# Kernel tuning notes

Measured on AMD Instinct MI355X. Metric: run time of the kernel, lower is better.

The kernel has to match this reference:

```python
import jax, jax.numpy as jnp
import numpy as np

N = 20000      # nodes per graph
E = 320000     # edges per graph (before self-loops)
G = 256        # graphs (strings) per side
VOCAB = 128    # NUMBER_EMBEDDINGS
D_IN = 128
HID = 64
H = 4
D_OUT = 128
NEG_SLOPE = 0.2  # PyG GATConv leaky_relu slope


def _gat(x, edge_index, W, att_s, att_d, bias, concat):
    """PyG GATConv: gather -> per-edge logits -> segment softmax over dst -> scatter.
    x: [N, F_in], W: [F_in, H*C], att_s/att_d: [H, C], bias: [H*C] or [C].
    Self-loops are added (PyG default add_self_loops=True)."""
    n = x.shape[0]
    h, c = att_s.shape
    loops = jnp.arange(n)
    src = jnp.concatenate([edge_index[0], loops])  # message sources j
    dst = jnp.concatenate([edge_index[1], loops])  # message targets i
    xh = (x @ W).reshape(n, h, c)                  # [N,H,C]
    a_s = jnp.einsum('nhc,hc->nh', xh, att_s)      # [N,H]
    a_d = jnp.einsum('nhc,hc->nh', xh, att_d)
    logits = jax.nn.leaky_relu(a_s[src] + a_d[dst], NEG_SLOPE)  # [E',H]
    m = jax.ops.segment_max(logits, dst, num_segments=n)
    m = jnp.where(jnp.isfinite(m), m, 0.0)
    e = jnp.exp(logits - m[dst])
    z = jax.ops.segment_sum(e, dst, num_segments=n)
    alpha = e / (z[dst] + 1e-16)                   # [E',H]
    msg = xh[src] * alpha[:, :, None]              # [E',H,C]
    out = jax.ops.segment_sum(msg, dst, num_segments=n)  # [N,H,C]
    out = out.reshape(n, h * c) if concat else out.mean(axis=1)
    return out + bias


def _encode(xi, ei, batch, emb, W1, as1, ad1, b1, lw1, lb1,
            W2, as2, ad2, b2, lw2, lb2, W3, as3, ad3, b3, lw3, lb3):
    e = emb[xi]  # [N, D_IN]
    x = jax.nn.relu(_gat(e, ei, W1, as1, ad1, b1, True) + e @ lw1 + lb1)
    x = jax.nn.relu(_gat(x, ei, W2, as2, ad2, b2, True) + x @ lw2 + lb2)
    x = _gat(x, ei, W3, as3, ad3, b3, False) + x @ lw3 + lb3  # [N, D_OUT]
    s = jax.ops.segment_sum(x, batch, num_segments=G)
    cnt = jax.ops.segment_sum(jnp.ones((x.shape[0],), x.dtype), batch, num_segments=G)
    return s / jnp.maximum(cnt, 1.0)[:, None]  # global_mean_pool -> [G, D_OUT]


def setup_inputs() -> dict:
    key = jax.random.key(0)
    ks = jax.random.split(key, 32)
    hc = H * HID  # 256
    def nrm(k, shape, scale=0.05):
        return jax.random.normal(k, shape, dtype=jnp.float32) * scale
    inp = {
        'x_l': jax.random.randint(ks[0], (N,), 0, VOCAB),
        'edge_l': jax.random.randint(ks[1], (2, E), 0, N),
        'batch_l': jnp.sort(jax.random.randint(ks[2], (N,), 0, G)),
        'x_r': jax.random.randint(ks[3], (N,), 0, VOCAB),
        'edge_r': jax.random.randint(ks[4], (2, E), 0, N),
        'batch_r': jnp.sort(jax.random.randint(ks[5], (N,), 0, G)),
        'emb': nrm(ks[6], (VOCAB, D_IN), 1.0),
        'W1': nrm(ks[7], (D_IN, hc)), 'as1': nrm(ks[8], (H, HID)), 'ad1': nrm(ks[9], (H, HID)),
        'b1': jnp.zeros((hc,), jnp.float32), 'lw1': nrm(ks[10], (D_IN, hc)), 'lb1': jnp.zeros((hc,), jnp.float32),
        'W2': nrm(ks[11], (hc, hc)), 'as2': nrm(ks[12], (H, HID)), 'ad2': nrm(ks[13], (H, HID)),
        'b2': jnp.zeros((hc,), jnp.float32), 'lw2': nrm(ks[14], (hc, hc)), 'lb2': jnp.zeros((hc,), jnp.float32),
        'W3': nrm(ks[15], (hc, H * D_OUT)), 'as3': nrm(ks[16], (H, D_OUT)), 'ad3': nrm(ks[17], (H, D_OUT)),
        'b3': jnp.zeros((D_OUT,), jnp.float32), 'lw3': nrm(ks[18], (hc, D_OUT)), 'lb3': jnp.zeros((D_OUT,), jnp.float32),
    }
    return inp


def reference(x_l, edge_l, batch_l, x_r, edge_r, batch_r, emb,
              W1, as1, ad1, b1, lw1, lb1,
              W2, as2, ad2, b2, lw2, lb2,
              W3, as3, ad3, b3, lw3, lb3):
    params = (emb, W1, as1, ad1, b1, lw1, lb1, W2, as2, ad2, b2, lw2, lb2,
              W3, as3, ad3, b3, lw3, lb3)
    out_l = _encode(x_l, edge_l, batch_l, *params)
    out_r = _encode(x_r, edge_r, batch_r, *params)
    return (out_l, out_r)
```

## Files before the change

kernel.cpp:

```cpp
#include <hip/hip_runtime.h>

#define GG 256

typedef __bf16 bf16x8 __attribute__((ext_vector_type(8)));
typedef __bf16 bf16x4 __attribute__((ext_vector_type(4)));
typedef float floatx4 __attribute__((ext_vector_type(4)));
typedef float f32x2 __attribute__((ext_vector_type(2)));

__device__ __forceinline__ float lrelu(float x) { return x > 0.f ? x : 0.2f * x; }

__device__ __forceinline__ int permM(int m) {
    int g = m >> 6, q = m & 63;
    return (g << 6) | ((q & 3) << 4) | (q >> 2);
}

__device__ __forceinline__ void wt1(const float* __restrict__ B, __bf16* __restrict__ Bt,
                                    int K, int M, int idx) {
    int k = idx / M, m = idx - k * M;
    Bt[(size_t)permM(m) * K + k] = (__bf16)B[idx];
}
__device__ __forceinline__ void wattn1(const float* __restrict__ W,
                                       const float* __restrict__ as_,
                                       const float* __restrict__ ad_,
                                       __bf16* __restrict__ dst, int K, int C, int idx) {
    int j = idx / K, k = idx - j * K;
    float v = 0.f;
    if (j < 8) {
        int h = j & 3;
        const float* att = (j < 4) ? as_ : ad_;
        int M = 4 * C;
        for (int c = 0; c < C; c++) v += W[(size_t)k * M + h * C + c] * att[h * C + c];
    }
    dst[(size_t)j * K + k] = (__bf16)v;
}

__global__ void k_wprep(const float* W1, const float* lw1, const float* as1, const float* ad1,
                        const float* W2, const float* lw2, const float* as2, const float* ad2,
                        const float* W3, const float* lw3, const float* as3, const float* ad3,
                        __bf16* B1t, __bf16* B2t, __bf16* B3t) {
    int idx = blockIdx.x * blockDim.x + threadIdx.x;
    if (idx < 32768) { wt1(W1, B1t, 128, 256, idx); return; }
    idx -= 32768;
    if (idx < 32768) { wt1(lw1, B1t + 256 * 128, 128, 256, idx); return; }
    idx -= 32768;
    if (idx < 2048) { wattn1(W1, as1, ad1, B1t + 512 * 128, 128, 64, idx); return; }
    idx -= 2048;
    if (idx < 65536) { wt1(W2, B2t, 256, 256, idx); return; }
    idx -= 65536;
    if (idx < 65536) { wt1(lw2, B2t + 256 * 256, 256, 256, idx); return; }
    idx -= 65536;
    if (idx < 4096) { wattn1(W2, as2, ad2, B2t + 512 * 256, 256, 64, idx); return; }
    idx -= 4096;
    if (idx < 131072) { wt1(W3, B3t, 256, 512, idx); return; }
    idx -= 131072;
    if (idx < 32768) { wt1(lw3, B3t + 512 * 256, 256, 128, idx); return; }
    idx -= 32768;
    if (idx < 4096) { wattn1(W3, as3, ad3, B3t + 640 * 256, 256, 128, idx); }
}

template <int K, bool EMB, bool LINBF>
__global__ __launch_bounds__(256) void k_gemm_all(const __bf16* __restrict__ A,
                                                  const int* __restrict__ xl,
                                                  const int* __restrict__ xr,
                                                  const float* __restrict__ emb,
                                                  const __bf16* __restrict__ Bt,
                                                  int n, int n1, int Mx, int Ml,
                                                  unsigned char* __restrict__ x8, int ldx,
                                                  float* __restrict__ linf,
                                                  __bf16* __restrict__ linb, int ldl,
                                                  const float* __restrict__ bias1,
                                                  const float* __restrict__ bias2,
                                                  float* __restrict__ a_s,
                                                  float* __restrict__ a_d) {
    constexpr int KS = K / 32;
    constexpr int LDK = K + 8;
    constexpr int LPR = K / 8;
    constexpr int NCH = 64 * LPR / 256;
    __shared__ __bf16 S[64 * LDK];
    int tid = threadIdx.x;
    int wave = tid >> 6, lane = tid & 63;
    int row0 = blockIdx.x * 64;
#pragma unroll
    for (int c = 0; c < NCH; c++) {
        int i = tid + c * 256;
        int r = i / LPR, ko = (i - r * LPR) * 8;
        int gr = row0 + r;
        bf16x8 v = {};
        if (gr < n) {
            if (EMB) {
                int xi = (gr < n1) ? xl[gr] : xr[gr - n1];
                const float4* src = (const float4*)(emb + ((size_t)xi << 7) + ko);
                float4 q0 = src[0], q1 = src[1];
                v = bf16x8{(__bf16)q0.x, (__bf16)q0.y, (__bf16)q0.z, (__bf16)q0.w,
                           (__bf16)q1.x, (__bf16)q1.y, (__bf16)q1.z, (__bf16)q1.w};
            } else {
                v = *(const bf16x8*)(A + (size_t)gr * K + ko);
            }
        }
        *(bf16x8*)&S[r * LDK + ko] = v;
    }
    __syncthreads();
    int kOff = (lane >> 4) * 8;
    int colBase = lane & 15;
    bf16x8 af[KS];
#pragma unroll
    for (int ks = 0; ks < KS; ks++)
        af[ks] = *(const bf16x8*)&S[(wave * 16 + colBase) * LDK + ks * 32 + kOff];
    int Mtot = Mx + Ml;
    int gr0 = row0 + wave * 16 + ((lane >> 4) << 2);
    int half = (Mtot / 128) * 64;
    int c0beg = blockIdx.y * half;
    int T = half / 64;
    bf16x8 regs[NCH];
#pragma unroll
    for (int c = 0; c < NCH; c++) {
        int i = tid + c * 256;
        int r = i / LPR, ko = (i - r * LPR) * 8;
        regs[c] = *(const bf16x8*)(Bt + (size_t)(c0beg + r) * K + ko);
    }
    for (int t = 0; t < T; t++) {
        __syncthreads();
#pragma unroll
        for (int c = 0; c < NCH; c++) {
            int i = tid + c * 256;
            int r = i / LPR, ko = (i - r * LPR) * 8;
            *(bf16x8*)&S[r * LDK + ko] = regs[c];
        }
        if (t + 1 < T) {
            int c0n = c0beg + (t + 1) * 64;
#pragma unroll
            for (int c = 0; c < NCH; c++) {
                int i = tid + c * 256;
                int r = i / LPR, ko = (i - r * LPR) * 8;
                regs[c] = *(const bf16x8*)(Bt + (size_t)(c0n + r) * K + ko);
            }
        }
        __syncthreads();
        floatx4 acc[4] = {};
#pragma unroll
        for (int ct = 0; ct < 4; ct++) {
#pragma unroll
            for (int ks = 0; ks < KS; ks++) {
                bf16x8 bf = *(const bf16x8*)&S[(ct * 16 + colBase) * LDK + ks * 32 + kOff];
                acc[ct] = __builtin_amdgcn_mfma_f32_16x16x32_bf16(af[ks], bf, acc[ct], 0, 0, 0);
            }
        }
        int c0 = c0beg + t * 64;
        if (c0 < Mx) {
#pragma unroll
            for (int r = 0; r < 4; r++) {
                int gr = gr0 + r;
                if (gr >= n) continue;
                int p = __builtin_amdgcn_cvt_pk_fp8_f32(acc[0][r], acc[1][r], 0, false);
                p = __builtin_amdgcn_cvt_pk_fp8_f32(acc[2][r], acc[3][r], p, true);
                *(unsigned int*)(x8 + (size_t)gr * ldx + c0 + colBase * 4) = (unsigned int)p;
            }
        } else {
            int c2 = c0 + colBase * 4 - Mx;
#pragma unroll
            for (int r = 0; r < 4; r++) {
                int gr = gr0 + r;
                if (gr >= n) continue;
                float v0 = acc[0][r] + bias1[c2 + 0];
                float v1 = acc[1][r] + bias1[c2 + 1];
                float v2 = acc[2][r] + bias1[c2 + 2];
                float v3 = acc[3][r] + bias1[c2 + 3];
                if (bias2) {
                    v0 += bias2[c2 + 0]; v1 += bias2[c2 + 1];
                    v2 += bias2[c2 + 2]; v3 += bias2[c2 + 3];
                }
                if (LINBF) {
                    bf16x4 o = {(__bf16)v0, (__bf16)v1, (__bf16)v2, (__bf16)v3};
                    *(bf16x4*)(linb + (size_t)gr * ldl + c2) = o;
                } else {
                    float4 o = {v0, v1, v2, v3};
                    *(float4*)(linf + (size_t)gr * ldl + c2) = o;
                }
            }
        }
    }
    if (blockIdx.y == 1) {
        floatx4 acc = {};
        const __bf16* bp = Bt + (size_t)(Mtot + colBase) * K + kOff;
#pragma unroll
        for (int ks = 0; ks < KS; ks++) {
            bf16x8 bf = *(const bf16x8*)(bp + ks * 32);
            acc = __builtin_amdgcn_mfma_f32_16x16x32_bf16(af[ks], bf, acc, 0, 0, 0);
        }
        if (colBase < 8) {
            float* dst = (colBase < 4) ? a_s : a_d;
            int h = colBase & 3;
#pragma unroll
            for (int r = 0; r < 4; r++) {
                int gr = gr0 + r;
                if (gr < n) dst[gr * 4 + h] = acc[r];
            }
        }
    }
}

__global__ void k_hist2(const int* __restrict__ el, const int* __restrict__ er,
                        int E, int n, int* __restrict__ deg) {
    int e = blockIdx.x * blockDim.x + threadIdx.x;
    if (e >= 2 * E) return;
    int d = (e < E) ? el[E + e] : er[E + (e - E)] + n;
    atomicAdd(&deg[d], 1);
}

__global__ __launch_bounds__(1024) void k_scan1(int* __restrict__ rp, int n,
                                                int* __restrict__ part) {
    __shared__ int wsum[16];
    int i = blockIdx.x * 1024 + threadIdx.x;
    int lane = threadIdx.x & 63, wid = threadIdx.x >> 6;
    int v = (i < n) ? rp[i] : 0;
    int inc = v;
#pragma unroll
    for (int off = 1; off < 64; off <<= 1) {
        int t = __shfl_up(inc, off, 64);
        if (lane >= off) inc += t;
    }
    if (lane == 63) wsum[wid] = inc;
    __syncthreads();
    if (wid == 0) {
        int wv = (lane < 16) ? wsum[lane] : 0;
        int winc = wv;
#pragma unroll
        for (int off = 1; off < 16; off <<= 1) {
            int t = __shfl_up(winc, off, 64);
            if (lane >= off) winc += t;
        }
        if (lane < 16) wsum[lane] = winc - wv;
        if (lane == 15) part[blockIdx.x] = winc;
    }
    __syncthreads();
    if (i < n) rp[i] = wsum[wid] + (inc - v);
}

__global__ void k_scan2(int* __restrict__ part, int nb) {
    int lane = threadIdx.x;
    int v = (lane < nb) ? part[lane] : 0;
    int inc = v;
#pragma unroll
    for (int off = 1; off < 64; off <<= 1) {
        int t = __shfl_up(inc, off, 64);
        if (lane >= off) inc += t;
    }
    if (lane < nb) part[lane] = inc - v;
}

__global__ __launch_bounds__(1024) void k_scan3(int* __restrict__ rp, int n,
                                                const int* __restrict__ part) {
    int i = blockIdx.x * 1024 + threadIdx.x;
    if (i < n) rp[i] += part[blockIdx.x];
}

__global__ void k_fill2(const int* __restrict__ el, const int* __restrict__ er,
                        int E, int n, int* __restrict__ rp, int* __restrict__ csr) {
    int e = blockIdx.x * blockDim.x + threadIdx.x;
    if (e >= 2 * E) return;
    int d, s;
    if (e < E) { s = el[e]; d = el[E + e]; }
    else       { s = er[e - E] + n; d = er[E + (e - E)] + n; }
    int pos = atomicAdd(&rp[d], 1);
    csr[pos] = s;
}

__device__ __forceinline__ void dec4(unsigned int u, float* f) {
    f32x2 a = __builtin_amdgcn_cvt_pk_f32_fp8(u, false);
    f32x2 b = __builtin_amdgcn_cvt_pk_f32_fp8(u, true);
    f[0] = a[0]; f[1] = a[1]; f[2] = b[0]; f[3] = b[1];
}

__device__ __forceinline__ int swz_block(int bid, int nbx) {
    if (nbx & 7) return bid;
    int halfb = nbx >> 1;
    int grp = bid >> 3, r = bid & 7;
    int j = grp * 4 + (r & 3);
    return (r < 4) ? j : halfb + j;
}

__global__ __launch_bounds__(256) void k_agg12(const int* __restrict__ rp,
                                               const int* __restrict__ csr,
                                               const float* __restrict__ a_s,
                                               const float* __restrict__ a_d,
                                               const unsigned char* __restrict__ x8,
                                               const __bf16* __restrict__ lin,
                                               __bf16* __restrict__ out_bf, int n) {
    int nb = swz_block(blockIdx.x, gridDim.x);
    int lane = threadIdx.x & 63;
    int half = lane >> 5, sl = lane & 31;
    int node = nb * 4 + (threadIdx.x >> 6);
    if (node >= n) return;
    int c0 = sl * 8;
    int h = sl >> 3;
    int start = node ? rp[node - 1] : 0;
    int end = rp[node];
    float ad = a_d[node * 4 + h];
    float z = 0.f;
    float acc[8] = {};
    if (half == 0) {
        z = __expf(lrelu(a_s[node * 4 + h] + ad));
        uint2 u = *(const uint2*)(x8 + (size_t)node * 256 + c0);
        float f[8];
        dec4(u.x, f); dec4(u.y, f + 4);
#pragma unroll
        for (int j = 0; j < 8; j++) acc[j] = z * f[j];
    }
    uint2 u0 = {}, u1 = {}, u2 = {};
    float A0 = 0.f, A1 = 0.f, A2 = 0.f;
    int e0 = start + half;
    if (e0 < end) {
        int s = csr[e0];
        u0 = *(const uint2*)(x8 + (size_t)s * 256 + c0);
        A0 = a_s[s * 4 + h];
    }
    if (e0 + 2 < end) {
        int s = csr[e0 + 2];
        u1 = *(const uint2*)(x8 + (size_t)s * 256 + c0);
        A1 = a_s[s * 4 + h];
    }
    if (e0 + 4 < end) {
        int s = csr[e0 + 4];
        u2 = *(const uint2*)(x8 + (size_t)s * 256 + c0);
        A2 = a_s[s * 4 + h];
    }
    for (int e = e0; e < end; e += 2) {
        uint2 uc = u0;
        float ac = A0;
        u0 = u1; A0 = A1;
        u1 = u2; A1 = A2;
        int pn = e + 6;
        pn = pn < end ? pn : end - 1;
        int s = csr[pn];
        u2 = *(const uint2*)(x8 + (size_t)s * 256 + c0);
        A2 = a_s[s * 4 + h];
        float w = __expf(lrelu(ac + ad));
        z += w;
        float f[8];
        dec4(uc.x, f); dec4(uc.y, f + 4);
#pragma unroll
        for (int q = 0; q < 8; q++) acc[q] += w * f[q];
    }
    z += __shfl_xor(z, 32, 64);
#pragma unroll
    for (int j = 0; j < 8; j++) acc[j] += __shfl_xor(acc[j], 32, 64);
    if (half == 0) {
        float inv = 1.f / (z + 1e-16f);
        bf16x8 l = *(const bf16x8*)(lin + (size_t)node * 256 + c0);
        bf16x8 r;
#pragma unroll
        for (int j = 0; j < 8; j++)
            r[j] = (__bf16)fmaxf(acc[j] * inv + (float)l[j], 0.f);
        *(bf16x8*)(out_bf + (size_t)node * 256 + c0) = r;
    }
}

__global__ __launch_bounds__(256) void k_agg3(const int* __restrict__ rp,
                                              const int* __restrict__ csr,
                                              const float* __restrict__ a_s,
                                              const float* __restrict__ a_d,
                                              const unsigned int* __restrict__ x8,
                                              float* __restrict__ mean, int n) {
    int nb = swz_block(blockIdx.x, gridDim.x);
    int lane = threadIdx.x & 63;
    int half = lane >> 5, sl = lane & 31;
    int node = nb * 4 + (threadIdx.x >> 6);
    if (node >= n) return;
    int h = sl >> 3;
    int start = node ? rp[node - 1] : 0;
    int end = rp[node];
    float ad = a_d[node * 4 + h];
    float z = 0.f;
    float acc[16] = {};
    if (half == 0) {
        z = __expf(lrelu(a_s[node * 4 + h] + ad));
        uint4 u = *(const uint4*)(x8 + (size_t)node * 128 + sl * 4);
        float f[16];
        dec4(u.x, f); dec4(u.y, f + 4); dec4(u.z, f + 8); dec4(u.w, f + 12);
#pragma unroll
        for (int j = 0; j < 16; j++) acc[j] = z * f[j];
    }
    uint4 u0 = {}, u1 = {}, u2 = {};
    float A0 = 0.f, A1 = 0.f, A2 = 0.f;
    int e0 = start + half;
    if (e0 < end) {
        int s = csr[e0];
        u0 = *(const uint4*)(x8 + (size_t)s * 128 + sl * 4);
        A0 = a_s[s * 4 + h];
    }
    if (e0 + 2 < end) {
        int s = csr[e0 + 2];
        u1 = *(const uint4*)(x8 + (size_t)s * 128 + sl * 4);
        A1 = a_s[s * 4 + h];
    }
    if (e0 + 4 < end) {
        int s = csr[e0 + 4];
        u2 = *(const uint4*)(x8 + (size_t)s * 128 + sl * 4);
        A2 = a_s[s * 4 + h];
    }
    for (int e = e0; e < end; e += 2) {
        uint4 uc = u0;
        float ac = A0;
        u0 = u1; A0 = A1;
        u1 = u2; A1 = A2;
        int pn = e + 6;
        pn = pn < end ? pn : end - 1;
        int s = csr[pn];
        u2 = *(const uint4*)(x8 + (size_t)s * 128 + sl * 4);
        A2 = a_s[s * 4 + h];
        float w = __expf(lrelu(ac + ad));
        z += w;
        float f[16];
        dec4(uc.x, f); dec4(uc.y, f + 4); dec4(uc.z, f + 8); dec4(uc.w, f + 12);
#pragma unroll
        for (int q = 0; q < 16; q++) acc[q] += w * f[q];
    }
    z += __shfl_xor(z, 32, 64);
#pragma unroll
    for (int j = 0; j < 16; j++) acc[j] += __shfl_xor(acc[j], 32, 64);
    float scale = 0.25f / (z + 1e-16f);
#pragma unroll
    for (int j = 0; j < 16; j++) {
        float v = acc[j] * scale;
        v += __shfl_xor(v, 8, 64);
        v += __shfl_xor(v, 16, 64);
        acc[j] = v;
    }
    if (lane < 8) {
        float4* op = (float4*)(mean + (size_t)node * 128 + lane * 16);
#pragma unroll
        for (int q = 0; q < 4; q++) {
            float4 o = {acc[4 * q], acc[4 * q + 1], acc[4 * q + 2], acc[4 * q + 3]};
            op[q] = o;
        }
    }
}

__global__ __launch_bounds__(128) void k_pool(const float* __restrict__ mean,
                                              const float* __restrict__ lin3,
                                              const float* __restrict__ b3,
                                              const int* __restrict__ bl,
                                              const int* __restrict__ br,
                                              int n, float* __restrict__ out) {
    int g = blockIdx.x, c = threadIdx.x;
    const int* b = (g < GG) ? bl : br;
    int tg = (g < GG) ? g : g - GG;
    int off = (g < GG) ? 0 : n;
    int s, e;
    { int lo = 0, hi = n; while (lo < hi) { int m = (lo + hi) >> 1; if (b[m] < tg) lo = m + 1; else hi = m; } s = lo; }
    { int lo = 0, hi = n; while (lo < hi) { int m = (lo + hi) >> 1; if (b[m] < tg + 1) lo = m + 1; else hi = m; } e = lo; }
    s += off; e += off;
    float acc = 0.f;
    for (int i = s; i < e; i++)
        acc += mean[(size_t)i * 128 + c] + lin3[(size_t)i * 128 + c];
    int cnt = e - s;
    out[(size_t)g * 128 + c] = cnt > 0 ? acc / (float)cnt + b3[c] : 0.f;
}

static inline int cdiv(int a, int b) { return (a + b - 1) / b; }

extern "C" void kernel_launch(void* const* d_in, const int* in_sizes, int n_in,
                              void* d_out, int out_size, void* d_ws, size_t ws_size,
                              hipStream_t stream) {
    const int* x_l = (const int*)d_in[0];
    const int* edge_l = (const int*)d_in[1];
    const int* batch_l = (const int*)d_in[2];
    const int* x_r = (const int*)d_in[3];
    const int* edge_r = (const int*)d_in[4];
    const int* batch_r = (const int*)d_in[5];
    const float* emb = (const float*)d_in[6];
    const float* W1 = (const float*)d_in[7];
    const float* as1 = (const float*)d_in[8];
    const float* ad1 = (const float*)d_in[9];
    const float* b1 = (const float*)d_in[10];
    const float* lw1 = (const float*)d_in[11];
    const float* lb1 = (const float*)d_in[12];
    const float* W2 = (const float*)d_in[13];
    const float* as2 = (const float*)d_in[14];
    const float* ad2 = (const float*)d_in[15];
    const float* b2 = (const float*)d_in[16];
    const float* lw2 = (const float*)d_in[17];
    const float* lb2 = (const float*)d_in[18];
    const float* W3 = (const float*)d_in[19];
    const float* as3 = (const float*)d_in[20];
    const float* ad3 = (const float*)d_in[21];
    const float* b3 = (const float*)d_in[22];
    const float* lw3 = (const float*)d_in[23];
    const float* lb3 = (const float*)d_in[24];

    const int n = in_sizes[0];
    const int E = in_sizes[1] / 2;
    const int N2 = 2 * n;
    const int NB = cdiv(N2, 1024);

    float* MEAN = (float*)d_ws;
    float* L3 = MEAN + (size_t)N2 * 128;
    float* a_s = L3 + (size_t)N2 * 128;
    float* a_d = a_s + (size_t)N2 * 4;
    int* rp = (int*)(a_d + (size_t)N2 * 4);
    int* csr = rp + N2;
    int* part = csr + 2 * E;
    __bf16* LINb = (__bf16*)(part + 64);
    unsigned char* X8a = (unsigned char*)(LINb + (size_t)N2 * 256);
    unsigned char* X8b = X8a + (size_t)N2 * 256;
    __bf16* Abf = (__bf16*)(X8b + (size_t)N2 * 512);
    __bf16* B1t = Abf + (size_t)N2 * 256;
    __bf16* B2t = B1t + 528 * 128;
    __bf16* B3t = B2t + 528 * 256;

    const int TB = 256;
    dim3 blk(TB);

    k_wprep<<<cdiv(370688, TB), blk, 0, stream>>>(W1, lw1, as1, ad1, W2, lw2, as2, ad2,
                                                  W3, lw3, as3, ad3, B1t, B2t, B3t);

    hipMemsetAsync(rp, 0, sizeof(int) * (size_t)N2, stream);
    k_hist2<<<cdiv(2 * E, TB), blk, 0, stream>>>(edge_l, edge_r, E, n, rp);
    k_scan1<<<NB, 1024, 0, stream>>>(rp, N2, part);
    k_scan2<<<1, 64, 0, stream>>>(part, NB);
    k_scan3<<<NB, 1024, 0, stream>>>(rp, N2, part);
    k_fill2<<<cdiv(2 * E, TB), blk, 0, stream>>>(edge_l, edge_r, E, n, rp, csr);

    k_gemm_all<128, true, true><<<dim3(cdiv(N2, 64), 2), blk, 0, stream>>>(
        nullptr, x_l, x_r, emb, B1t, N2, n, 256, 256, X8a, 256, nullptr, LINb, 256, lb1, b1, a_s, a_d);
    k_agg12<<<cdiv(N2, 4), blk, 0, stream>>>(rp, csr, a_s, a_d, X8a, LINb, Abf, N2);

    k_gemm_all<256, false, true><<<dim3(cdiv(N2, 64), 2), blk, 0, stream>>>(
        Abf, nullptr, nullptr, nullptr, B2t, N2, n, 256, 256, X8a, 256, nullptr, LINb, 256, lb2, b2, a_s, a_d);
    k_agg12<<<cdiv(N2, 4), blk, 0, stream>>>(rp, csr, a_s, a_d, X8a, LINb, Abf, N2);

    k_gemm_all<256, false, false><<<dim3(cdiv(N2, 64), 2), blk, 0, stream>>>(
        Abf, nullptr, nullptr, nullptr, B3t, N2, n, 512, 128, X8b, 512, L3, nullptr, 128, lb3, nullptr, a_s, a_d);
    k_agg3<<<cdiv(N2, 4), blk, 0, stream>>>(rp, csr, a_s, a_d, (const unsigned int*)X8b, MEAN, N2);
    k_pool<<<2 * GG, 128, 0, stream>>>(MEAN, L3, b3, batch_l, batch_r, n, (float*)d_out);
}
```

Measured before the change: 447.5 us.

## Double GEMM row tile to 128 and load A fragments directly from global

The fused GEMM now gives each block 128 rows instead of 64, so every wave holds two 16-row A fragments and reuses each B tile in shared memory across twice as many MFMAs. The A tile is read straight from global memory (or the embedding table) into registers, removing the shared-memory staging pass and its barrier. The aim is to halve B-tile global and LDS traffic per output row and to cut block count. The cost is higher register pressure from doubled accumulators and fragments, which may lower occupancy, and fewer blocks across the device.

Result: no change. 455.7 us (+1.8%).

```diff
diff --git a/kernel.cpp b/kernel.cpp
--- a/kernel.cpp
+++ b/kernel.cpp
@@ -79,35 +79,34 @@
     __shared__ __bf16 S[64 * LDK];
     int tid = threadIdx.x;
     int wave = tid >> 6, lane = tid & 63;
-    int row0 = blockIdx.x * 64;
-#pragma unroll
-    for (int c = 0; c < NCH; c++) {
-        int i = tid + c * 256;
-        int r = i / LPR, ko = (i - r * LPR) * 8;
-        int gr = row0 + r;
-        bf16x8 v = {};
-        if (gr < n) {
-            if (EMB) {
-                int xi = (gr < n1) ? xl[gr] : xr[gr - n1];
-                const float4* src = (const float4*)(emb + ((size_t)xi << 7) + ko);
-                float4 q0 = src[0], q1 = src[1];
-                v = bf16x8{(__bf16)q0.x, (__bf16)q0.y, (__bf16)q0.z, (__bf16)q0.w,
-                           (__bf16)q1.x, (__bf16)q1.y, (__bf16)q1.z, (__bf16)q1.w};
-            } else {
-                v = *(const bf16x8*)(A + (size_t)gr * K + ko);
-            }
-        }
-        *(bf16x8*)&S[r * LDK + ko] = v;
-    }
-    __syncthreads();
+    int row0 = blockIdx.x * 128;
     int kOff = (lane >> 4) * 8;
     int colBase = lane & 15;
-    bf16x8 af[KS];
-#pragma unroll
-    for (int ks = 0; ks < KS; ks++)
-        af[ks] = *(const bf16x8*)&S[(wave * 16 + colBase) * LDK + ks * 32 + kOff];
+
+    bf16x8 af[2][KS];
+#pragma unroll
+    for (int as = 0; as < 2; as++) {
+        int row = row0 + wave * 32 + as * 16 + colBase;
+        row = row < n ? row : (n - 1);
+        if (EMB) {
+            int xi = (row < n1) ? xl[row] : xr[row - n1];
+            const float* src = emb + ((size_t)xi << 7);
+#pragma unroll
+            for (int ks = 0; ks < KS; ks++) {
+                const float4* p = (const float4*)(src + ks * 32 + kOff);
+                float4 q0 = p[0], q1 = p[1];
+                af[as][ks] = bf16x8{(__bf16)q0.x, (__bf16)q0.y, (__bf16)q0.z, (__bf16)q0.w,
+                                    (__bf16)q1.x, (__bf16)q1.y, (__bf16)q1.z, (__bf16)q1.w};
+            }
+        } else {
+            const __bf16* src = A + (size_t)row * K;
+#pragma unroll
+            for (int ks = 0; ks < KS; ks++)
+                af[as][ks] = *(const bf16x8*)(src + ks * 32 + kOff);
+        }
+    }
+
     int Mtot = Mx + Ml;
-    int gr0 = row0 + wave * 16 + ((lane >> 4) << 2);
     int half = (Mtot / 128) * 64;
     int c0beg = blockIdx.y * half;
     int T = half / 64;
@@ -136,64 +135,72 @@
             }
         }
         __syncthreads();
-        floatx4 acc[4] = {};
+        floatx4 acc[2][4] = {};
 #pragma unroll
         for (int ct = 0; ct < 4; ct++) {
 #pragma unroll
             for (int ks = 0; ks < KS; ks++) {
                 bf16x8 bf = *(const bf16x8*)&S[(ct * 16 + colBase) * LDK + ks * 32 + kOff];
-                acc[ct] = __builtin_amdgcn_mfma_f32_16x16x32_bf16(af[ks], bf, acc[ct], 0, 0, 0);
+                acc[0][ct] = __builtin_amdgcn_mfma_f32_16x16x32_bf16(af[0][ks], bf, acc[0][ct], 0, 0, 0);
+                acc[1][ct] = __builtin_amdgcn_mfma_f32_16x16x32_bf16(af[1][ks], bf, acc[1][ct], 0, 0, 0);
             }
         }
         int c0 = c0beg + t * 64;
-        if (c0 < Mx) {
-#pragma unroll
-            for (int r = 0; r < 4; r++) {
-                int gr = gr0 + r;
-                if (gr >= n) continue;
-                int p = __builtin_amdgcn_cvt_pk_fp8_f32(acc[0][r], acc[1][r], 0, false);
-                p = __builtin_amdgcn_cvt_pk_fp8_f32(acc[2][r], acc[3][r], p, true);
-                *(unsigned int*)(x8 + (size_t)gr * ldx + c0 + colBase * 4) = (unsigned int)p;
-            }
-        } else {
-            int c2 = c0 + colBase * 4 - Mx;
-#pragma unroll
-            for (int r = 0; r < 4; r++) {
-                int gr = gr0 + r;
-                if (gr >= n) continue;
-                float v0 = acc[0][r] + bias1[c2 + 0];
-                float v1 = acc[1][r] + bias1[c2 + 1];
-                float v2 = acc[2][r] + bias1[c2 + 2];
-                float v3 = acc[3][r] + bias1[c2 + 3];
-                if (bias2) {
-                    v0 += bias2[c2 + 0]; v1 += bias2[c2 + 1];
-                    v2 += bias2[c2 + 2]; v3 += bias2[c2 + 3];
+#pragma unroll
+        for (int as = 0; as < 2; as++) {
+            int gr0 = row0 + wave * 32 + as * 16 + ((lane >> 4) << 2);
+            if (c0 < Mx) {
+#pragma unroll
+                for (int r = 0; r < 4; r++) {
+                    int gr = gr0 + r;
+                    if (gr >= n) continue;
+                    int p = __builtin_amdgcn_cvt_pk_fp8_f32(acc[as][0][r], acc[as][1][r], 0, false);
+                    p = __builtin_amdgcn_cvt_pk_fp8_f32(acc[as][2][r], acc[as][3][r], p, true);
+                    *(unsigned int*)(x8 + (size_t)gr * ldx + c0 + colBase * 4) = (unsigned int)p;
                 }
-                if (LINBF) {
-                    bf16x4 o = {(__bf16)v0, (__bf16)v1, (__bf16)v2, (__bf16)v3};
-                    *(bf16x4*)(linb + (size_t)gr * ldl + c2) = o;
-                } else {
-                    float4 o = {v0, v1, v2, v3};
-                    *(float4*)(linf + (size_t)gr * ldl + c2) = o;
+            } else {
+                int c2 = c0 + colBase * 4 - Mx;
+#pragma unroll
+                for (int r = 0; r < 4; r++) {
+                    int gr = gr0 + r;
+                    if (gr >= n) continue;
+                    float v0 = acc[as][0][r] + bias1[c2 + 0];
+                    float v1 = acc[as][1][r] + bias1[c2 + 1];
+                    float v2 = acc[as][2][r] + bias1[c2 + 2];
+                    float v3 = acc[as][3][r] + bias1[c2 + 3];
+                    if (bias2) {
+                        v0 += bias2[c2 + 0]; v1 += bias2[c2 + 1];
+                        v2 += bias2[c2 + 2]; v3 += bias2[c2 + 3];
+                    }
+                    if (LINBF) {
+                        bf16x4 o = {(__bf16)v0, (__bf16)v1, (__bf16)v2, (__bf16)v3};
+                        *(bf16x4*)(linb + (size_t)gr * ldl + c2) = o;
+                    } else {
+                        float4 o = {v0, v1, v2, v3};
+                        *(float4*)(linf + (size_t)gr * ldl + c2) = o;
+                    }
                 }
             }
         }
     }
     if (blockIdx.y == 1) {
-        floatx4 acc = {};
         const __bf16* bp = Bt + (size_t)(Mtot + colBase) * K + kOff;
 #pragma unroll
-        for (int ks = 0; ks < KS; ks++) {
-            bf16x8 bf = *(const bf16x8*)(bp + ks * 32);
-            acc = __builtin_amdgcn_mfma_f32_16x16x32_bf16(af[ks], bf, acc, 0, 0, 0);
-        }
-        if (colBase < 8) {
-            float* dst = (colBase < 4) ? a_s : a_d;
-            int h = colBase & 3;
-#pragma unroll
-            for (int r = 0; r < 4; r++) {
-                int gr = gr0 + r;
-                if (gr < n) dst[gr * 4 + h] = acc[r];
+        for (int as = 0; as < 2; as++) {
+            floatx4 acc = {};
+#pragma unroll
+            for (int ks = 0; ks < KS; ks++) {
+                bf16x8 bf = *(const bf16x8*)(bp + ks * 32);
+                acc = __builtin_amdgcn_mfma_f32_16x16x32_bf16(af[as][ks], bf, acc, 0, 0, 0);
+            }
+            if (colBase < 8) {
+                float* dst = (colBase < 4) ? a_s : a_d;
+                int h = colBase & 3;
+#pragma unroll
+                for (int r = 0; r < 4; r++) {
+                    int gr = row0 + wave * 32 + as * 16 + ((lane >> 4) << 2) + r;
+                    if (gr < n) dst[gr * 4 + h] = acc[r];
+                }
             }
         }
     }
@@ -521,15 +528,15 @@
     k_scan3<<<NB, 1024, 0, stream>>>(rp, N2, part);
     k_fill2<<<cdiv(2 * E, TB), blk, 0, stream>>>(edge_l, edge_r, E, n, rp, csr);
 
-    k_gemm_all<128, true, true><<<dim3(cdiv(N2, 64), 2), blk, 0, stream>>>(
+    k_gemm_all<128, true, true><<<dim3(cdiv(N2, 128), 2), blk, 0, stream>>>(
         nullptr, x_l, x_r, emb, B1t, N2, n, 256, 256, X8a, 256, nullptr, LINb, 256, lb1, b1, a_s, a_d);
     k_agg12<<<cdiv(N2, 4), blk, 0, stream>>>(rp, csr, a_s, a_d, X8a, LINb, Abf, N2);
 
-    k_gemm_all<256, false, true><<<dim3(cdiv(N2, 64), 2), blk, 0, stream>>>(
+    k_gemm_all<256, false, true><<<dim3(cdiv(N2, 128), 2), blk, 0, stream>>>(
         Abf, nullptr, nullptr, nullptr, B2t, N2, n, 256, 256, X8a, 256, nullptr, LINb, 256, lb2, b2, a_s, a_d);
     k_agg12<<<cdiv(N2, 4), blk, 0, stream>>>(rp, csr, a_s, a_d, X8a, LINb, Abf, N2);
 
-    k_gemm_all<256, false, false><<<dim3(cdiv(N2, 64), 2), blk, 0, stream>>>(
+    k_gemm_all<256, false, false><<<dim3(cdiv(N2, 128), 2), blk, 0, stream>>>(
         Abf, nullptr, nullptr, nullptr, B3t, N2, n, 512, 128, X8b, 512, L3, nullptr, 128, lb3, nullptr, a_s, a_d);
     k_agg3<<<cdiv(N2, 4), blk, 0, stream>>>(rp, csr, a_s, a_d, (const unsigned int*)X8b, MEAN, N2);
     k_pool<<<2 * GG, 128, 0, stream>>>(MEAN, L3, b3, batch_l, batch_r, n, (float*)d_out);
```
